# Optimization experiments

Measured on AMD Instinct MI355X. Metric: run time of the kernel, lower is better.

## Reference

```python
import jax, jax.numpy as jnp
import numpy as np

N = 500_000   # total nodes across the batch of graphs
D = 256       # node feature dim
G = 4096      # number of graphs (segments)


def setup_inputs() -> dict:
    key = jax.random.key(0)
    k1, k2, k3 = jax.random.split(key, 3)
    x = jax.random.normal(k1, (N, D), dtype=jnp.float32)
    batch = jnp.sort(jax.random.randint(k2, (N,), 0, G, dtype=jnp.int64))
    Wg = jax.random.normal(k3, (D,), dtype=jnp.float32) * (1.0 / np.sqrt(D))
    bg = jnp.zeros((1,), dtype=jnp.float32)
    return {"x": x, "batch": batch, "Wg": Wg, "bg": bg}


def reference(x, batch, Wg, bg):
    # gate_nn: Linear(D, 1), then squeeze -> [N]
    gate = x @ Wg + bg[0]
    # scatter_softmax over segments defined by batch
    gmax = jax.ops.segment_max(gate, batch, num_segments=G, indices_are_sorted=True)
    e = jnp.exp(gate - gmax[batch])
    denom = jax.ops.segment_sum(e, batch, num_segments=G, indices_are_sorted=True)
    attn = e / denom[batch]
    # weighted scatter-add pooling -> [G, D]
    out = jax.ops.segment_sum(x * attn[:, None], batch, num_segments=G,
                              indices_are_sorted=True)
    return out
```

## Files before the change

kernel.cpp:

```cpp
#include <hip/hip_runtime.h>
#include <math.h>


#define DIM 256
#define RCHUNK 8

__device__ __forceinline__ int lower_bound(const int* __restrict__ b, int n, int key) {
    int lo = 0, hi = n;
    while (lo < hi) {
        int mid = (lo + hi) >> 1;
        if (b[mid] < key) lo = mid + 1; else hi = mid;
    }
    return lo;
}

__global__ __launch_bounds__(256)
void gap_fused_kernel(const float* __restrict__ x,
                      const int* __restrict__ batch,
                      const float* __restrict__ Wg,
                      const float* __restrict__ bg,
                      float* __restrict__ out,
                      int N) {
    const int g   = blockIdx.x;
    const int tid = threadIdx.x;

    const int start = lower_bound(batch, N, g);
    const int end   = lower_bound(batch, N, g + 1);

    __shared__ float s_rows[RCHUNK * DIM];
    __shared__ float s_gates[RCHUNK];

    if (start >= end) {
        out[(size_t)g * DIM + tid] = 0.0f;
        return;
    }

    const int lane = tid & 63;
    const int wv   = tid >> 6;
    const float4 wgv  = ((const float4*)Wg)[lane];
    const float  bias = bg[0];

    const int len = end - start;
    const float4* __restrict__ x4 = (const float4*)x + (size_t)start * (DIM / 4);
    float4* s4 = (float4*)s_rows;

    float m = -INFINITY;
    float l = 0.0f;
    float acc = 0.0f;

    for (int c = 0; c < len; c += RCHUNK) {
        __syncthreads();

        const int r0 = c + wv;
        const int r1 = c + wv + 4;
        float g0 = -INFINITY, g1 = -INFINITY;

        if (r0 < len) {
            float4 v = x4[(size_t)r0 * 64 + lane];
            s4[wv * 64 + lane] = v;
            float d = fmaf(v.x, wgv.x, fmaf(v.y, wgv.y, fmaf(v.z, wgv.z, v.w * wgv.w)));
            #pragma unroll
            for (int off = 32; off; off >>= 1) d += __shfl_xor(d, off);
            g0 = d + bias;
        } else {
            s4[wv * 64 + lane] = make_float4(0.f, 0.f, 0.f, 0.f);
        }
        if (r1 < len) {
            float4 v = x4[(size_t)r1 * 64 + lane];
            s4[(wv + 4) * 64 + lane] = v;
            float d = fmaf(v.x, wgv.x, fmaf(v.y, wgv.y, fmaf(v.z, wgv.z, v.w * wgv.w)));
            #pragma unroll
            for (int off = 32; off; off >>= 1) d += __shfl_xor(d, off);
            g1 = d + bias;
        } else {
            s4[(wv + 4) * 64 + lane] = make_float4(0.f, 0.f, 0.f, 0.f);
        }
        if (lane == 0) {
            s_gates[wv]     = g0;
            s_gates[wv + 4] = g1;
        }
        __syncthreads();

        float gl[RCHUNK];
        float cmax = -INFINITY;
        #pragma unroll
        for (int i = 0; i < RCHUNK; ++i) {
            gl[i] = s_gates[i];
            cmax = fmaxf(cmax, gl[i]);
        }
        const float nm    = fmaxf(m, cmax);
        const float alpha = __expf(m - nm);
        acc *= alpha;
        l   *= alpha;
        #pragma unroll
        for (int i = 0; i < RCHUNK; ++i) {
            const float p = __expf(gl[i] - nm);
            l += p;
            acc = fmaf(p, s_rows[i * DIM + tid], acc);
        }
        m = nm;
    }

    out[(size_t)g * DIM + tid] = acc / l;
}

extern "C" void kernel_launch(void* const* d_in, const int* in_sizes, int n_in,
                              void* d_out, int out_size, void* d_ws, size_t ws_size,
                              hipStream_t stream) {
    const float* x     = (const float*)d_in[0];
    const int*   batch = (const int*)d_in[1];
    const float* Wg    = (const float*)d_in[2];
    const float* bg    = (const float*)d_in[3];
    float*       out   = (float*)d_out;

    const int N = in_sizes[1];
    const int G = out_size / DIM;

    gap_fused_kernel<<<G, DIM, 0, stream>>>(x, batch, Wg, bg, out, N);
}
```

Baseline: 668.7 us.

## Keep per-wave online softmax state in registers and merge waves at end

Each wavefront now streams its own rows and keeps an independent online-softmax max, sum and float4 accumulator in registers. The per-chunk shared-memory staging of rows and gates is gone, along with the two block barriers per 8-row chunk. The four wave partials are combined once at the end through shared memory with a rescale by the global max. This removes repeated barrier stalls and LDS traffic in what is meant to be a bandwidth-bound loop, at the cost of more registers and a final merge step.

```diff
diff --git a/kernel.cpp b/kernel.cpp
--- a/kernel.cpp
+++ b/kernel.cpp
@@ -3,7 +3,6 @@
 
 
 #define DIM 256
-#define RCHUNK 8
 
 __device__ __forceinline__ int lower_bound(const int* __restrict__ b, int n, int key) {
     int lo = 0, hi = n;
@@ -21,87 +20,73 @@
                       const float* __restrict__ bg,
                       float* __restrict__ out,
                       int N) {
-    const int g   = blockIdx.x;
-    const int tid = threadIdx.x;
+    const int g    = blockIdx.x;
+    const int tid  = threadIdx.x;
+    const int lane = tid & 63;
+    const int wv   = tid >> 6;
 
     const int start = lower_bound(batch, N, g);
     const int end   = lower_bound(batch, N, g + 1);
 
-    __shared__ float s_rows[RCHUNK * DIM];
-    __shared__ float s_gates[RCHUNK];
+    __shared__ float s_ml[8];
+    __shared__ float s_acc[4 * DIM];
 
     if (start >= end) {
         out[(size_t)g * DIM + tid] = 0.0f;
         return;
     }
 
-    const int lane = tid & 63;
-    const int wv   = tid >> 6;
     const float4 wgv  = ((const float4*)Wg)[lane];
     const float  bias = bg[0];
+    const int    len  = end - start;
+    const float4* __restrict__ x4 = (const float4*)x + (size_t)start * (DIM / 4);
 
-    const int len = end - start;
-    const float4* __restrict__ x4 = (const float4*)x + (size_t)start * (DIM / 4);
-    float4* s4 = (float4*)s_rows;
+    float  m   = -INFINITY;
+    float  l   = 0.0f;
+    float4 acc = make_float4(0.f, 0.f, 0.f, 0.f);
 
-    float m = -INFINITY;
-    float l = 0.0f;
-    float acc = 0.0f;
+    for (int r = wv; r < len; r += 8) {
+        const int  r2   = r + 4;
+        const bool has2 = (r2 < len);
+        float4 v0 = x4[(size_t)r * 64 + lane];
+        float4 v1 = make_float4(0.f, 0.f, 0.f, 0.f);
+        if (has2) v1 = x4[(size_t)r2 * 64 + lane];
 
-    for (int c = 0; c < len; c += RCHUNK) {
-        __syncthreads();
+        float d0 = fmaf(v0.x, wgv.x, fmaf(v0.y, wgv.y, fmaf(v0.z, wgv.z, v0.w * wgv.w)));
+        float d1 = fmaf(v1.x, wgv.x, fmaf(v1.y, wgv.y, fmaf(v1.z, wgv.z, v1.w * wgv.w)));
+        #pragma unroll
+        for (int off = 32; off; off >>= 1) {
+            d0 += __shfl_xor(d0, off);
+            d1 += __shfl_xor(d1, off);
+        }
+        const float g0 = d0 + bias;
+        const float g1 = has2 ? (d1 + bias) : -INFINITY;
 
-        const int r0 = c + wv;
-        const int r1 = c + wv + 4;
-        float g0 = -INFINITY, g1 = -INFINITY;
-
-        if (r0 < len) {
-            float4 v = x4[(size_t)r0 * 64 + lane];
-            s4[wv * 64 + lane] = v;
-            float d = fmaf(v.x, wgv.x, fmaf(v.y, wgv.y, fmaf(v.z, wgv.z, v.w * wgv.w)));
-            #pragma unroll
-            for (int off = 32; off; off >>= 1) d += __shfl_xor(d, off);
-            g0 = d + bias;
-        } else {
-            s4[wv * 64 + lane] = make_float4(0.f, 0.f, 0.f, 0.f);
-        }
-        if (r1 < len) {
-            float4 v = x4[(size_t)r1 * 64 + lane];
-            s4[(wv + 4) * 64 + lane] = v;
-            float d = fmaf(v.x, wgv.x, fmaf(v.y, wgv.y, fmaf(v.z, wgv.z, v.w * wgv.w)));
-            #pragma unroll
-            for (int off = 32; off; off >>= 1) d += __shfl_xor(d, off);
-            g1 = d + bias;
-        } else {
-            s4[(wv + 4) * 64 + lane] = make_float4(0.f, 0.f, 0.f, 0.f);
-        }
-        if (lane == 0) {
-            s_gates[wv]     = g0;
-            s_gates[wv + 4] = g1;
-        }
-        __syncthreads();
-
-        float gl[RCHUNK];
-        float cmax = -INFINITY;
-        #pragma unroll
-        for (int i = 0; i < RCHUNK; ++i) {
-            gl[i] = s_gates[i];
-            cmax = fmaxf(cmax, gl[i]);
-        }
-        const float nm    = fmaxf(m, cmax);
+        const float nm    = fmaxf(m, fmaxf(g0, g1));
         const float alpha = __expf(m - nm);
-        acc *= alpha;
-        l   *= alpha;
-        #pragma unroll
-        for (int i = 0; i < RCHUNK; ++i) {
-            const float p = __expf(gl[i] - nm);
-            l += p;
-            acc = fmaf(p, s_rows[i * DIM + tid], acc);
-        }
+        const float p0    = __expf(g0 - nm);
+        const float p1    = __expf(g1 - nm);
+        l = fmaf(l, alpha, p0 + p1);
+        acc.x = fmaf(p0, v0.x, fmaf(p1, v1.x, acc.x * alpha));
+        acc.y = fmaf(p0, v0.y, fmaf(p1, v1.y, acc.y * alpha));
+        acc.z = fmaf(p0, v0.z, fmaf(p1, v1.z, acc.z * alpha));
+        acc.w = fmaf(p0, v0.w, fmaf(p1, v1.w, acc.w * alpha));
         m = nm;
     }
 
-    out[(size_t)g * DIM + tid] = acc / l;
+    if (lane == 0) { s_ml[wv] = m; s_ml[4 + wv] = l; }
+    ((float4*)s_acc)[wv * 64 + lane] = acc;
+    __syncthreads();
+
+    const float M = fmaxf(fmaxf(s_ml[0], s_ml[1]), fmaxf(s_ml[2], s_ml[3]));
+    float denom = 0.f, val = 0.f;
+    #pragma unroll
+    for (int w = 0; w < 4; ++w) {
+        const float sc = __expf(s_ml[w] - M);
+        denom = fmaf(s_ml[4 + w], sc, denom);
+        val   = fmaf(s_acc[w * DIM + tid], sc, val);
+    }
+    out[(size_t)g * DIM + tid] = val / denom;
 }
 
 extern "C" void kernel_launch(void* const* d_in, const int* in_sizes, int n_in,
```

Result: no change. 660.5 us (-1.2%).
